# Performance work log

Measured on AMD Instinct MI355X. Metric: run time of the kernel, lower is better.

## Reference

```python
import jax, jax.numpy as jnp
import numpy as np

N = 50000; E = 800000
GNN_IN = 256; MLP_IN = 256; HID = 512; F_DIM = 128; H = 2; NCLS = 40
HC = H * F_DIM  # 256


def setup_inputs() -> dict:
    key = jax.random.key(0)
    ks = jax.random.split(key, 24)
    w = lambda k, shape: (jax.random.normal(k, shape, jnp.float32) * 0.05)
    inp = {
        'x_gsage': jax.random.normal(ks[0], (N, GNN_IN), jnp.float32),
        'edge_index': jax.random.randint(ks[1], (2, E), 0, N),
        'x_mlp': jax.random.normal(ks[2], (N, MLP_IN), jnp.float32),
        # TransformerConv params (query/key/value/skip linears)
        'Wq': w(ks[3], (HC, GNN_IN)), 'bq': jnp.zeros(HC, jnp.float32),
        'Wk': w(ks[4], (HC, GNN_IN)), 'bk': jnp.zeros(HC, jnp.float32),
        'Wv': w(ks[5], (HC, GNN_IN)), 'bv': jnp.zeros(HC, jnp.float32),
        'Wskip': w(ks[6], (HC, GNN_IN)), 'bskip': jnp.zeros(HC, jnp.float32),
        # MLP (num_layers=3): in->hid, hid->hid, hid->2*F_DIM; 2 batchnorms
        'W1': w(ks[7], (HID, MLP_IN)), 'b1': jnp.zeros(HID, jnp.float32),
        'g1': jnp.ones(HID, jnp.float32), 'be1': jnp.zeros(HID, jnp.float32),
        'W2': w(ks[8], (HID, HID)), 'b2': jnp.zeros(HID, jnp.float32),
        'g2': jnp.ones(HID, jnp.float32), 'be2': jnp.zeros(HID, jnp.float32),
        'W3': w(ks[9], (HC, HID)), 'b3': jnp.zeros(HC, jnp.float32),
        # fusion scalars
        'alpha': jnp.array([0.5], jnp.float32), 'beta': jnp.array([0.5], jnp.float32),
        # classifier head
        'Wc1': w(ks[10], (HID, HC)), 'bc1': jnp.zeros(HID, jnp.float32),
        'Wc2': w(ks[11], (NCLS, HID)), 'bc2': jnp.zeros(NCLS, jnp.float32),
    }
    return inp


def _lin(x, W, b):
    return x @ W.T + b


def _batchnorm(x, g, b, eps=1e-5):
    mu = jnp.mean(x, axis=0)
    var = jnp.var(x, axis=0)
    return (x - mu) * jax.lax.rsqrt(var + eps) * g + b


def _transformer_conv(x, edge_index, Wq, bq, Wk, bk, Wv, bv, Wskip, bskip):
    # PyG TransformerConv, heads=H, concat=True, root_weight=True (eval: no dropout)
    q = _lin(x, Wq, bq).reshape(N, H, F_DIM)
    k = _lin(x, Wk, bk).reshape(N, H, F_DIM)
    v = _lin(x, Wv, bv).reshape(N, H, F_DIM)
    src, dst = edge_index[0], edge_index[1]
    # per-edge, per-head attention logits  [E, H]
    logits = jnp.einsum('ehd,ehd->eh', q[dst], k[src]) / jnp.sqrt(jnp.float32(F_DIM))
    # segment softmax over incoming edges of each destination node
    amax = jax.ops.segment_max(logits, dst, num_segments=N)  # [N, H]
    amax = jnp.where(jnp.isfinite(amax), amax, 0.0)
    ex = jnp.exp(logits - amax[dst])                           # [E, H]
    denom = jax.ops.segment_sum(ex, dst, num_segments=N)      # [N, H]
    attn = ex / jnp.maximum(denom[dst], 1e-16)                 # [E, H]
    msg = v[src] * attn[:, :, None]                            # [E, H, C]
    out = jax.ops.segment_sum(msg, dst, num_segments=N)       # [N, H, C]
    out = out.reshape(N, HC) + _lin(x, Wskip, bskip)
    return out


def reference(x_gsage, edge_index, x_mlp, Wq, bq, Wk, bk, Wv, bv, Wskip, bskip,
              W1, b1, g1, be1, W2, b2, g2, be2, W3, b3, alpha, beta,
              Wc1, bc1, Wc2, bc2):
    h_g = _transformer_conv(x_gsage, edge_index, Wq, bq, Wk, bk, Wv, bv, Wskip, bskip)
    # MLP branch: (lin -> BN(batch stats) -> sigmoid) x2, then final lin; dropout off (eval)
    h = jax.nn.sigmoid(_batchnorm(_lin(x_mlp, W1, b1), g1, be1))
    h = jax.nn.sigmoid(_batchnorm(_lin(h, W2, b2), g2, be2))
    h_m = _lin(h, W3, b3)
    h_fused = alpha * h_g + beta * h_m
    out = _lin(jax.nn.relu(_lin(h_fused, Wc1, bc1)), Wc2, bc2)
    return out
```

## Files before the change

kernel.cpp:

```cpp
#include <hip/hip_runtime.h>
#include <hip/hip_bf16.h>
#include <cstdint>
#include <cstddef>

typedef __attribute__((ext_vector_type(8))) short short8;
typedef __attribute__((ext_vector_type(4))) float f32x4;

__device__ inline ushort f2bs(float f) {
    __hip_bfloat16 h = __float2bfloat16(f);
    return *(ushort*)&h;
}
__device__ inline float bu2f(ushort u) {
    return __uint_as_float(((unsigned)u) << 16);
}

template <int AB, int BM, int KT>
__global__ __launch_bounds__(256) void gemm_fullk(
    const void* __restrict__ Avoid, const short* __restrict__ Wb,
    const float* __restrict__ bias, ushort* __restrict__ C,
    int M, int NT, int act)
{
    __shared__ short As[BM][KT + 8];
    __shared__ short Bs[128][40];

    const int tid = threadIdx.x;
    const int lane = tid & 63;
    const int w = tid >> 6;
    const int wm = w >> 1, wn = w & 1;
    constexpr int MI = BM / 32;
    const int m0 = blockIdx.x * BM;
    const int lr = lane & 15;
    const int lk = (lane >> 4) * 8;
    const int Ntot = NT * 128;

    {
        constexpr int TPR = KT / 128;
        const int arow = tid / TPR;
        const int ac0 = (tid % TPR) * 128;
        const bool ok = (m0 + arow) < M;
        if (AB == 0) {
            const float* ap = (const float*)Avoid + (size_t)(m0 + arow) * KT + ac0;
#pragma unroll
            for (int j = 0; j < 16; ++j) {
                float4 x = ok ? *(const float4*)(ap + j * 8)
                              : make_float4(0.f, 0.f, 0.f, 0.f);
                float4 y = ok ? *(const float4*)(ap + j * 8 + 4)
                              : make_float4(0.f, 0.f, 0.f, 0.f);
                short8 v;
                v[0] = f2bs(x.x); v[1] = f2bs(x.y); v[2] = f2bs(x.z); v[3] = f2bs(x.w);
                v[4] = f2bs(y.x); v[5] = f2bs(y.y); v[6] = f2bs(y.z); v[7] = f2bs(y.w);
                *(short8*)&As[arow][ac0 + j * 8] = v;
            }
        } else {
            const short* ap = (const short*)Avoid + (size_t)(m0 + arow) * KT + ac0;
#pragma unroll
            for (int j = 0; j < 16; ++j) {
                short8 v = {};
                if (ok) v = *(const short8*)(ap + j * 8);
                *(short8*)&As[arow][ac0 + j * 8] = v;
            }
        }
    }

    const int trow = tid >> 1;
    const int tcg = (tid & 1) * 16;

    f32x4 acc[MI][4] = {};

    for (int t = 0; t < NT; ++t) {
        for (int k0 = 0; k0 < KT; k0 += 32) {
            const short* wp = Wb + (size_t)(t * 128 + trow) * KT + k0 + tcg;
            *(short8*)&Bs[trow][tcg] = *(const short8*)wp;
            *(short8*)&Bs[trow][tcg + 8] = *(const short8*)(wp + 8);
            __syncthreads();

            short8 afr[MI], bfr[4];
#pragma unroll
            for (int mi = 0; mi < MI; ++mi)
                afr[mi] = *(const short8*)&As[wm * (BM / 2) + mi * 16 + lr][k0 + lk];
#pragma unroll
            for (int nj = 0; nj < 4; ++nj)
                bfr[nj] = *(const short8*)&Bs[wn * 64 + nj * 16 + lr][lk];
#pragma unroll
            for (int mi = 0; mi < MI; ++mi)
#pragma unroll
                for (int nj = 0; nj < 4; ++nj)
                    acc[mi][nj] = __builtin_amdgcn_mfma_f32_16x16x32_bf16(
                        afr[mi], bfr[nj], acc[mi][nj], 0, 0, 0);
            __syncthreads();
        }
#pragma unroll
        for (int mi = 0; mi < MI; ++mi) {
#pragma unroll
            for (int nj = 0; nj < 4; ++nj) {
                int gn = t * 128 + wn * 64 + nj * 16 + lr;
                float b = bias[gn];
#pragma unroll
                for (int r = 0; r < 4; ++r) {
                    int gm = m0 + wm * (BM / 2) + mi * 16 + (lane >> 4) * 4 + r;
                    if (gm < M) {
                        float v = acc[mi][nj][r] + b;
                        if (act == 1) v = fmaxf(v, 0.f);
                        C[(size_t)gm * Ntot + gn] = f2bs(v);
                    }
                }
                acc[mi][nj] = (f32x4){0.f, 0.f, 0.f, 0.f};
            }
        }
    }
}

__global__ __launch_bounds__(256) void mfma_gemm_small(
    const short* __restrict__ A, const float* __restrict__ W,
    const float* __restrict__ bias, float* __restrict__ Cf,
    int M, int K, int Nout)
{
    __shared__ short As[128][40];
    __shared__ short Bs[128][40];
    const int tid = threadIdx.x;
    const int lane = tid & 63;
    const int w = tid >> 6;
    const int wm = w >> 1, wn = w & 1;
    const int m0 = blockIdx.y * 128, n0 = blockIdx.x * 128;
    const int trow = tid >> 1;
    const int tcg = (tid & 1) * 16;
    const int lr = lane & 15;
    const int lk = (lane >> 4) * 8;

    f32x4 acc[4][4] = {};

    for (int k0 = 0; k0 < K; k0 += 32) {
        {
            bool ok = (m0 + trow) < M;
            const short* ap = A + (size_t)(m0 + trow) * K + k0 + tcg;
            short8 s0 = {}, s1 = {};
            if (ok) { s0 = *(const short8*)(ap); s1 = *(const short8*)(ap + 8); }
            *(short8*)&As[trow][tcg] = s0;
            *(short8*)&As[trow][tcg + 8] = s1;
        }
        {
            short v[16];
            bool ok = (n0 + trow) < Nout;
            const float* wp = W + (size_t)(n0 + trow) * K + k0 + tcg;
#pragma unroll
            for (int q = 0; q < 4; ++q) {
                float4 t4 = ok ? *(const float4*)(wp + q * 4)
                               : make_float4(0.f, 0.f, 0.f, 0.f);
                v[q * 4 + 0] = f2bs(t4.x); v[q * 4 + 1] = f2bs(t4.y);
                v[q * 4 + 2] = f2bs(t4.z); v[q * 4 + 3] = f2bs(t4.w);
            }
            short8 w0, w1;
#pragma unroll
            for (int j = 0; j < 8; ++j) { w0[j] = v[j]; w1[j] = v[j + 8]; }
            *(short8*)&Bs[trow][tcg] = w0;
            *(short8*)&Bs[trow][tcg + 8] = w1;
        }
        __syncthreads();
        short8 afr[4], bfr[4];
#pragma unroll
        for (int mi = 0; mi < 4; ++mi)
            afr[mi] = *(const short8*)&As[wm * 64 + mi * 16 + lr][lk];
#pragma unroll
        for (int nj = 0; nj < 4; ++nj)
            bfr[nj] = *(const short8*)&Bs[wn * 64 + nj * 16 + lr][lk];
#pragma unroll
        for (int mi = 0; mi < 4; ++mi)
#pragma unroll
            for (int nj = 0; nj < 4; ++nj)
                acc[mi][nj] = __builtin_amdgcn_mfma_f32_16x16x32_bf16(
                    afr[mi], bfr[nj], acc[mi][nj], 0, 0, 0);
        __syncthreads();
    }
#pragma unroll
    for (int mi = 0; mi < 4; ++mi)
#pragma unroll
        for (int nj = 0; nj < 4; ++nj) {
            int gn = n0 + wn * 64 + nj * 16 + lr;
            if (gn >= Nout) continue;
            float b = bias[gn];
#pragma unroll
            for (int r = 0; r < 4; ++r) {
                int gm = m0 + wm * 64 + mi * 16 + (lane >> 4) * 4 + r;
                if (gm < M) Cf[(size_t)gm * Nout + gn] = acc[mi][nj][r] + b;
            }
        }
}

__global__ void zero_words(unsigned* __restrict__ p, size_t n)
{
    size_t i = (size_t)blockIdx.x * blockDim.x + threadIdx.x;
    size_t stride = (size_t)gridDim.x * blockDim.x;
    for (; i < n; i += stride) p[i] = 0u;
}

__global__ void cvt_f32_bf16(const float* __restrict__ s, ushort* __restrict__ d,
                             size_t n4)
{
    size_t i = (size_t)blockIdx.x * blockDim.x + threadIdx.x;
    size_t stride = (size_t)gridDim.x * blockDim.x;
    for (; i < n4; i += stride) {
        float4 v = ((const float4*)s)[i];
        ushort4 o;
        o.x = f2bs(v.x); o.y = f2bs(v.y); o.z = f2bs(v.z); o.w = f2bs(v.w);
        ((ushort4*)d)[i] = o;
    }
}

__global__ void copy_f32(const float* __restrict__ s, float* __restrict__ d, int n)
{
    int i = blockIdx.x * blockDim.x + threadIdx.x;
    if (i < n) d[i] = s[i];
}

__global__ __launch_bounds__(256) void bn_stats512_b(
    const ushort* __restrict__ X, float* __restrict__ sums,
    float* __restrict__ sumsq, int M)
{
    int t = threadIdx.x;
    float s0 = 0.f, q0 = 0.f, s1 = 0.f, q1 = 0.f;
    for (int r = blockIdx.x; r < M; r += gridDim.x) {
        ushort2 v = *(const ushort2*)(X + (size_t)r * 512 + 2 * t);
        float a = bu2f(v.x), b = bu2f(v.y);
        s0 += a; q0 += a * a;
        s1 += b; q1 += b * b;
    }
    atomicAdd(&sums[2 * t], s0);
    atomicAdd(&sumsq[2 * t], q0);
    atomicAdd(&sums[2 * t + 1], s1);
    atomicAdd(&sumsq[2 * t + 1], q1);
}

__global__ void bn_finalize(const float* __restrict__ sums,
                            const float* __restrict__ sumsq,
                            const float* __restrict__ g,
                            const float* __restrict__ be,
                            float* __restrict__ scale, float* __restrict__ shift,
                            int M, int C)
{
    int c = blockIdx.x * blockDim.x + threadIdx.x;
    if (c >= C) return;
    float mean = sums[c] / (float)M;
    float var = sumsq[c] / (float)M - mean * mean;
    float inv = rsqrtf(var + 1e-5f);
    float sc = g[c] * inv;
    scale[c] = sc;
    shift[c] = be[c] - mean * sc;
}

__global__ void bn_apply_sig4(ushort* __restrict__ X,
                              const float* __restrict__ scale,
                              const float* __restrict__ shift, size_t n4)
{
    size_t i = (size_t)blockIdx.x * blockDim.x + threadIdx.x;
    size_t stride = (size_t)gridDim.x * blockDim.x;
    for (; i < n4; i += stride) {
        ushort4 v = ((ushort4*)X)[i];
        int c0 = (int)((i * 4) & 511);
        float x0 = bu2f(v.x) * scale[c0] + shift[c0];
        float x1 = bu2f(v.y) * scale[c0 + 1] + shift[c0 + 1];
        float x2 = bu2f(v.z) * scale[c0 + 2] + shift[c0 + 2];
        float x3 = bu2f(v.w) * scale[c0 + 3] + shift[c0 + 3];
        v.x = f2bs(1.f / (1.f + __expf(-x0)));
        v.y = f2bs(1.f / (1.f + __expf(-x1)));
        v.z = f2bs(1.f / (1.f + __expf(-x2)));
        v.w = f2bs(1.f / (1.f + __expf(-x3)));
        ((ushort4*)X)[i] = v;
    }
}

__global__ void count_edges(const int* __restrict__ ei, int* __restrict__ counts, int E)
{
    int i = blockIdx.x * 256 + threadIdx.x;
    if (i < E) atomicAdd(&counts[ei[E + i]], 1);
}

__global__ __launch_bounds__(256) void scan_local(
    const int* __restrict__ cnt, int* __restrict__ excl,
    int* __restrict__ bsums, int n)
{
    __shared__ int s[256];
    int t = threadIdx.x;
    int i = blockIdx.x * 256 + t;
    int v = (i < n) ? cnt[i] : 0;
    s[t] = v;
    __syncthreads();
    for (int off = 1; off < 256; off <<= 1) {
        int u = (t >= off) ? s[t - off] : 0;
        __syncthreads();
        s[t] += u;
        __syncthreads();
    }
    if (i < n) excl[i] = s[t] - v;
    if (t == 255) bsums[blockIdx.x] = s[255];
}

__global__ __launch_bounds__(256) void scan_top(int* __restrict__ bsums, int nb)
{
    __shared__ int s[256];
    int t = threadIdx.x;
    int v = (t < nb) ? bsums[t] : 0;
    s[t] = v;
    __syncthreads();
    for (int off = 1; off < 256; off <<= 1) {
        int u = (t >= off) ? s[t - off] : 0;
        __syncthreads();
        s[t] += u;
        __syncthreads();
    }
    if (t < nb) bsums[t] = s[t] - v;
}

__global__ void scan_add(int* __restrict__ excl, const int* __restrict__ bsums,
                         int* __restrict__ cursor, int n)
{
    int i = blockIdx.x * 256 + threadIdx.x;
    if (i < n) {
        int v = excl[i] + bsums[blockIdx.x];
        excl[i] = v;
        cursor[i] = v;
    }
}

__global__ void fill_edges(const int* __restrict__ ei, int* __restrict__ cursor,
                           int* __restrict__ esrc, int E)
{
    int i = blockIdx.x * 256 + threadIdx.x;
    if (i < E) {
        int dst = ei[E + i];
        int pos = atomicAdd(&cursor[dst], 1);
        esrc[pos] = ei[i];
    }
}

__global__ __launch_bounds__(256) void edge_attn(
    const int* __restrict__ esrc, const int* __restrict__ offs,
    const int* __restrict__ cnts, const ushort* __restrict__ QKVS,
    const ushort* __restrict__ hmb, const float* __restrict__ alpha,
    const float* __restrict__ beta, ushort* __restrict__ hf, int N)
{
    int node = blockIdx.x * 4 + (threadIdx.x >> 6);
    int lane = threadIdx.x & 63;
    if (node >= N) return;
    int start = offs[node];
    int cnt = cnts[node];

    ushort4 qu = *(const ushort4*)(QKVS + (size_t)node * 1024 + lane * 4);
    float qx = bu2f(qu.x), qy = bu2f(qu.y), qz = bu2f(qu.z), qw = bu2f(qu.w);
    const float s = 0.088388347648318447f;

    float m = -INFINITY, d = 0.f;
    float a0 = 0.f, a1 = 0.f, a2 = 0.f, a3 = 0.f;

    ushort4 ku_n = {}, vu_n = {};
    if (cnt > 0) {
        int src0 = esrc[start];
        ku_n = *(const ushort4*)(QKVS + (size_t)src0 * 1024 + 256 + lane * 4);
        vu_n = *(const ushort4*)(QKVS + (size_t)src0 * 1024 + 512 + lane * 4);
    }
    for (int i = 0; i < cnt; ++i) {
        ushort4 ku = ku_n, vu = vu_n;
        if (i + 1 < cnt) {
            int srcn = esrc[start + i + 1];
            ku_n = *(const ushort4*)(QKVS + (size_t)srcn * 1024 + 256 + lane * 4);
            vu_n = *(const ushort4*)(QKVS + (size_t)srcn * 1024 + 512 + lane * 4);
        }
        float p = qx * bu2f(ku.x) + qy * bu2f(ku.y)
                + qz * bu2f(ku.z) + qw * bu2f(ku.w);
        p += __shfl_xor(p, 1);
        p += __shfl_xor(p, 2);
        p += __shfl_xor(p, 4);
        p += __shfl_xor(p, 8);
        p += __shfl_xor(p, 16);
        float l = p * s;
        float mn = fmaxf(m, l);
        float sc = __expf(m - mn);
        float pe = __expf(l - mn);
        d = d * sc + pe;
        a0 = a0 * sc + pe * bu2f(vu.x);
        a1 = a1 * sc + pe * bu2f(vu.y);
        a2 = a2 * sc + pe * bu2f(vu.z);
        a3 = a3 * sc + pe * bu2f(vu.w);
        m = mn;
    }
    float invd = (cnt > 0) ? 1.f / fmaxf(d, 1e-16f) : 0.f;
    float o0 = a0 * invd, o1 = a1 * invd, o2 = a2 * invd, o3 = a3 * invd;

    ushort4 su = *(const ushort4*)(QKVS + (size_t)node * 1024 + 768 + lane * 4);
    ushort4 hm = *(const ushort4*)(hmb + (size_t)node * 256 + lane * 4);
    float al = alpha[0], be = beta[0];
    ushort4 o;
    o.x = f2bs(al * (o0 + bu2f(su.x)) + be * bu2f(hm.x));
    o.y = f2bs(al * (o1 + bu2f(su.y)) + be * bu2f(hm.y));
    o.z = f2bs(al * (o2 + bu2f(su.z)) + be * bu2f(hm.z));
    o.w = f2bs(al * (o3 + bu2f(su.w)) + be * bu2f(hm.w));
    *(ushort4*)(hf + (size_t)node * 256 + lane * 4) = o;
}

extern "C" void kernel_launch(void* const* d_in, const int* in_sizes, int n_in,
                              void* d_out, int out_size, void* d_ws, size_t ws_size,
                              hipStream_t stream)
{
    const float* x_g   = (const float*)d_in[0];
    const int*   ei    = (const int*)d_in[1];
    const float* x_m   = (const float*)d_in[2];
    const float* Wq    = (const float*)d_in[3];
    const float* bq    = (const float*)d_in[4];
    const float* Wk    = (const float*)d_in[5];
    const float* bk    = (const float*)d_in[6];
    const float* Wv    = (const float*)d_in[7];
    const float* bv    = (const float*)d_in[8];
    const float* Wskip = (const float*)d_in[9];
    const float* bskip = (const float*)d_in[10];
    const float* W1    = (const float*)d_in[11];
    const float* b1    = (const float*)d_in[12];
    const float* g1    = (const float*)d_in[13];
    const float* be1   = (const float*)d_in[14];
    const float* W2    = (const float*)d_in[15];
    const float* b2    = (const float*)d_in[16];
    const float* g2    = (const float*)d_in[17];
    const float* be2   = (const float*)d_in[18];
    const float* W3    = (const float*)d_in[19];
    const float* b3    = (const float*)d_in[20];
    const float* alpha = (const float*)d_in[21];
    const float* beta  = (const float*)d_in[22];
    const float* Wc1   = (const float*)d_in[23];
    const float* bc1   = (const float*)d_in[24];
    const float* Wc2   = (const float*)d_in[25];
    const float* bc2   = (const float*)d_in[26];
    float* out = (float*)d_out;

    const int N = in_sizes[0] / 256;
    const int E = in_sizes[1] / 2;

    float* ws = (float*)d_ws;
    ushort* QKVS = (ushort*)ws;
    ushort* bufA = (ushort*)(ws + (size_t)N * 512);
    ushort* bufB = (ushort*)(ws + (size_t)N * 512 + (size_t)N * 256);
    ushort* hmb  = (ushort*)(ws + (size_t)N * 512 + 2 * (size_t)N * 256);
    float* wz = ws + (size_t)N * 512 + 2 * (size_t)N * 256 + (size_t)N * 128;

    float* sum1 = wz, *sq1 = wz + 512, *sum2 = wz + 1024, *sq2 = wz + 1536;
    int* counts = (int*)(wz + 2048);
    float* wz2 = wz + 2048 + N;
    float* scale1 = wz2, *shift1 = wz2 + 512;
    float* scale2 = wz2 + 1024, *shift2 = wz2 + 1536;
    int* bsums = (int*)(wz2 + 2048);
    int* offs = bsums + 256;
    int* cursor = offs + N;
    int* esrc = cursor + N;
    short* Wcat = (short*)(esrc + E);
    float* bcat = (float*)(Wcat + 1024 * 256);
    short* W1b  = (short*)(bcat + 1024);
    short* W2b  = W1b + 512 * 256;
    short* W3b  = W2b + 512 * 512;
    short* Wc1b = W3b + 256 * 512;

    dim3 blk(256);
    auto cvt = [&](const float* s, short* d, size_t n) {
        size_t n4 = n / 4;
        int g = (int)((n4 + 255) / 256);
        if (g > 512) g = 512;
        hipLaunchKernelGGL(cvt_f32_bf16, dim3(g), blk, 0, stream, s, (ushort*)d, n4);
    };

    hipLaunchKernelGGL(zero_words, dim3(128), blk, 0, stream,
                       (unsigned*)wz, (size_t)(2048 + N));

    cvt(Wq, Wcat, 256 * 256);
    cvt(Wk, Wcat + 256 * 256, 256 * 256);
    cvt(Wv, Wcat + 512 * 256, 256 * 256);
    cvt(Wskip, Wcat + 768 * 256, 256 * 256);
    cvt(W1, W1b, 512 * 256);
    cvt(W2, W2b, 512 * 512);
    cvt(W3, W3b, 256 * 512);
    cvt(Wc1, Wc1b, 512 * 256);
    hipLaunchKernelGGL(copy_f32, dim3(1), blk, 0, stream, bq, bcat, 256);
    hipLaunchKernelGGL(copy_f32, dim3(1), blk, 0, stream, bk, bcat + 256, 256);
    hipLaunchKernelGGL(copy_f32, dim3(1), blk, 0, stream, bv, bcat + 512, 256);
    hipLaunchKernelGGL(copy_f32, dim3(1), blk, 0, stream, bskip, bcat + 768, 256);

    const int nb = (N + 255) / 256;
    hipLaunchKernelGGL(count_edges, dim3((E + 255) / 256), blk, 0, stream, ei, counts, E);
    hipLaunchKernelGGL(scan_local, dim3(nb), blk, 0, stream, counts, offs, bsums, N);
    hipLaunchKernelGGL(scan_top, dim3(1), blk, 0, stream, bsums, nb);
    hipLaunchKernelGGL(scan_add, dim3(nb), blk, 0, stream, offs, bsums, cursor, N);
    hipLaunchKernelGGL(fill_edges, dim3((E + 255) / 256), blk, 0, stream, ei, cursor, esrc, E);

    const int g128 = (N + 127) / 128;
    const int g64 = (N + 63) / 64;

    hipLaunchKernelGGL((gemm_fullk<0, 128, 256>), dim3(g128), blk, 0, stream,
                       x_m, W1b, b1, bufA, N, 4, 0);
    hipLaunchKernelGGL(bn_stats512_b, dim3(512), blk, 0, stream, bufA, sum1, sq1, N);
    hipLaunchKernelGGL(bn_finalize, dim3(2), blk, 0, stream, sum1, sq1, g1, be1, scale1, shift1, N, 512);
    hipLaunchKernelGGL(bn_apply_sig4, dim3(2048), blk, 0, stream, bufA, scale1, shift1, (size_t)N * 128);
    hipLaunchKernelGGL((gemm_fullk<1, 64, 512>), dim3(g64), blk, 0, stream,
                       bufA, W2b, b2, bufB, N, 4, 0);
    hipLaunchKernelGGL(bn_stats512_b, dim3(512), blk, 0, stream, bufB, sum2, sq2, N);
    hipLaunchKernelGGL(bn_finalize, dim3(2), blk, 0, stream, sum2, sq2, g2, be2, scale2, shift2, N, 512);
    hipLaunchKernelGGL(bn_apply_sig4, dim3(2048), blk, 0, stream, bufB, scale2, shift2, (size_t)N * 128);
    hipLaunchKernelGGL((gemm_fullk<1, 64, 512>), dim3(g64), blk, 0, stream,
                       bufB, W3b, b3, hmb, N, 2, 0);

    hipLaunchKernelGGL((gemm_fullk<0, 128, 256>), dim3(g128), blk, 0, stream,
                       x_g, Wcat, bcat, QKVS, N, 8, 0);

    hipLaunchKernelGGL(edge_attn, dim3((N + 3) / 4), blk, 0, stream,
                       esrc, offs, counts, QKVS, hmb, alpha, beta, bufA, N);

    hipLaunchKernelGGL((gemm_fullk<1, 128, 256>), dim3(g128), blk, 0, stream,
                       bufA, Wc1b, bc1, bufB, N, 4, 1);
    hipLaunchKernelGGL(mfma_gemm_small, dim3(1, (N + 127) / 128), blk, 0, stream,
                       (const short*)bufB, Wc2, bc2, out, N, 512, 40);
}
```

Measured before the change: 940.9 us.

## Fuse BN+sigmoid into GEMM A-load, prefetch weights, pack param conversion

Removes the two standalone batchnorm-apply+sigmoid passes by applying scale/shift and sigmoid while staging A tiles into shared memory in the following GEMM. The GEMM loop is flattened over N-tiles and K-chunks, and the next weight chunk is prefetched into registers before the MFMA work so global loads overlap compute. The many small weight-convert and bias-copy launches are merged into one pack_params kernel. This saves two full read-write passes over 50000x512 bf16 buffers plus several launches, at the cost of extra per-element exp work inside the GEMM A-load.

New measurement: 962.6 us. 1.02x slower.

```diff
diff --git a/kernel.cpp b/kernel.cpp
--- a/kernel.cpp
+++ b/kernel.cpp
@@ -14,12 +14,14 @@
     return __uint_as_float(((unsigned)u) << 16);
 }
 
-template <int AB, int BM, int KT>
+template <int AB, int BM, int KT, int SIG>
 __global__ __launch_bounds__(256) void gemm_fullk(
     const void* __restrict__ Avoid, const short* __restrict__ Wb,
     const float* __restrict__ bias, ushort* __restrict__ C,
+    const float* __restrict__ scale, const float* __restrict__ shift,
     int M, int NT, int act)
 {
+    constexpr int KQ = KT / 32;
     __shared__ short As[BM][KT + 8];
     __shared__ short Bs[128][40];
 
@@ -57,6 +59,14 @@
             for (int j = 0; j < 16; ++j) {
                 short8 v = {};
                 if (ok) v = *(const short8*)(ap + j * 8);
+                if (SIG) {
+#pragma unroll
+                    for (int e = 0; e < 8; ++e) {
+                        int c = ac0 + j * 8 + e;
+                        float f = bu2f((ushort)v[e]) * scale[c] + shift[c];
+                        v[e] = (short)f2bs(1.f / (1.f + __expf(-f)));
+                    }
+                }
                 *(short8*)&As[arow][ac0 + j * 8] = v;
             }
         }
@@ -65,46 +75,64 @@
     const int trow = tid >> 1;
     const int tcg = (tid & 1) * 16;
 
+    short8 r0, r1;
+    {
+        const short* wp = Wb + (size_t)trow * KT + tcg;
+        r0 = *(const short8*)wp;
+        r1 = *(const short8*)(wp + 8);
+    }
+
     f32x4 acc[MI][4] = {};
-
-    for (int t = 0; t < NT; ++t) {
-        for (int k0 = 0; k0 < KT; k0 += 32) {
-            const short* wp = Wb + (size_t)(t * 128 + trow) * KT + k0 + tcg;
-            *(short8*)&Bs[trow][tcg] = *(const short8*)wp;
-            *(short8*)&Bs[trow][tcg + 8] = *(const short8*)(wp + 8);
-            __syncthreads();
-
-            short8 afr[MI], bfr[4];
-#pragma unroll
-            for (int mi = 0; mi < MI; ++mi)
-                afr[mi] = *(const short8*)&As[wm * (BM / 2) + mi * 16 + lr][k0 + lk];
+    const int total = NT * KQ;
+
+    for (int idx = 0; idx < total; ++idx) {
+        *(short8*)&Bs[trow][tcg] = r0;
+        *(short8*)&Bs[trow][tcg + 8] = r1;
+        __syncthreads();
+
+        const int nidx = idx + 1;
+        if (nidx < total) {
+            const int nt = nidx / KQ, nk = (nidx % KQ) * 32;
+            const short* wp = Wb + (size_t)(nt * 128 + trow) * KT + nk + tcg;
+            r0 = *(const short8*)wp;
+            r1 = *(const short8*)(wp + 8);
+        }
+
+        const int k0 = (idx % KQ) * 32;
+        short8 afr[MI], bfr[4];
+#pragma unroll
+        for (int mi = 0; mi < MI; ++mi)
+            afr[mi] = *(const short8*)&As[wm * (BM / 2) + mi * 16 + lr][k0 + lk];
+#pragma unroll
+        for (int nj = 0; nj < 4; ++nj)
+            bfr[nj] = *(const short8*)&Bs[wn * 64 + nj * 16 + lr][lk];
+#pragma unroll
+        for (int mi = 0; mi < MI; ++mi)
 #pragma unroll
             for (int nj = 0; nj < 4; ++nj)
-                bfr[nj] = *(const short8*)&Bs[wn * 64 + nj * 16 + lr][lk];
-#pragma unroll
-            for (int mi = 0; mi < MI; ++mi)
-#pragma unroll
-                for (int nj = 0; nj < 4; ++nj)
-                    acc[mi][nj] = __builtin_amdgcn_mfma_f32_16x16x32_bf16(
-                        afr[mi], bfr[nj], acc[mi][nj], 0, 0, 0);
-            __syncthreads();
-        }
-#pragma unroll
-        for (int mi = 0; mi < MI; ++mi) {
-#pragma unroll
-            for (int nj = 0; nj < 4; ++nj) {
-                int gn = t * 128 + wn * 64 + nj * 16 + lr;
-                float b = bias[gn];
-#pragma unroll
-                for (int r = 0; r < 4; ++r) {
-                    int gm = m0 + wm * (BM / 2) + mi * 16 + (lane >> 4) * 4 + r;
-                    if (gm < M) {
-                        float v = acc[mi][nj][r] + b;
-                        if (act == 1) v = fmaxf(v, 0.f);
-                        C[(size_t)gm * Ntot + gn] = f2bs(v);
+                acc[mi][nj] = __builtin_amdgcn_mfma_f32_16x16x32_bf16(
+                    afr[mi], bfr[nj], acc[mi][nj], 0, 0, 0);
+        __syncthreads();
+
+        if ((idx % KQ) == KQ - 1) {
+            const int t = idx / KQ;
+#pragma unroll
+            for (int mi = 0; mi < MI; ++mi) {
+#pragma unroll
+                for (int nj = 0; nj < 4; ++nj) {
+                    int gn = t * 128 + wn * 64 + nj * 16 + lr;
+                    float b = bias[gn];
+#pragma unroll
+                    for (int r = 0; r < 4; ++r) {
+                        int gm = m0 + wm * (BM / 2) + mi * 16 + (lane >> 4) * 4 + r;
+                        if (gm < M) {
+                            float v = acc[mi][nj][r] + b;
+                            if (act == 1) v = fmaxf(v, 0.f);
+                            C[(size_t)gm * Ntot + gn] = f2bs(v);
+                        }
                     }
+                    acc[mi][nj] = (f32x4){0.f, 0.f, 0.f, 0.f};
                 }
-                acc[mi][nj] = (f32x4){0.f, 0.f, 0.f, 0.f};
             }
         }
     }
@@ -193,23 +221,35 @@
     for (; i < n; i += stride) p[i] = 0u;
 }
 
-__global__ void cvt_f32_bf16(const float* __restrict__ s, ushort* __restrict__ d,
-                             size_t n4)
-{
-    size_t i = (size_t)blockIdx.x * blockDim.x + threadIdx.x;
-    size_t stride = (size_t)gridDim.x * blockDim.x;
-    for (; i < n4; i += stride) {
-        float4 v = ((const float4*)s)[i];
+__global__ void pack_params(
+    const float* __restrict__ Wq, const float* __restrict__ Wk,
+    const float* __restrict__ Wv, const float* __restrict__ Wskip,
+    const float* __restrict__ W1, const float* __restrict__ W2,
+    const float* __restrict__ W3, const float* __restrict__ Wc1,
+    const float* __restrict__ bq, const float* __restrict__ bk,
+    const float* __restrict__ bv, const float* __restrict__ bskip,
+    ushort* __restrict__ Wall, float* __restrict__ bcat)
+{
+    int q = blockIdx.x * 256 + threadIdx.x;
+    if (q < 229376) {
+        const float* s; int base4;
+        if      (q < 16384)  { s = Wq;    base4 = 0; }
+        else if (q < 32768)  { s = Wk;    base4 = 16384; }
+        else if (q < 49152)  { s = Wv;    base4 = 32768; }
+        else if (q < 65536)  { s = Wskip; base4 = 49152; }
+        else if (q < 98304)  { s = W1;    base4 = 65536; }
+        else if (q < 163840) { s = W2;    base4 = 98304; }
+        else if (q < 196608) { s = W3;    base4 = 163840; }
+        else                 { s = Wc1;   base4 = 196608; }
+        float4 v = ((const float4*)s)[q - base4];
         ushort4 o;
         o.x = f2bs(v.x); o.y = f2bs(v.y); o.z = f2bs(v.z); o.w = f2bs(v.w);
-        ((ushort4*)d)[i] = o;
-    }
-}
-
-__global__ void copy_f32(const float* __restrict__ s, float* __restrict__ d, int n)
-{
-    int i = blockIdx.x * blockDim.x + threadIdx.x;
-    if (i < n) d[i] = s[i];
+        ((ushort4*)Wall)[q] = o;
+    } else if (q < 229632) {
+        int j = q - 229376;
+        const float* s = (j < 64) ? bq : (j < 128) ? bk : (j < 192) ? bv : bskip;
+        ((float4*)bcat)[j] = ((const float4*)s)[j & 63];
+    }
 }
 
 __global__ __launch_bounds__(256) void bn_stats512_b(
@@ -245,27 +285,6 @@
     float sc = g[c] * inv;
     scale[c] = sc;
     shift[c] = be[c] - mean * sc;
-}
-
-__global__ void bn_apply_sig4(ushort* __restrict__ X,
-                              const float* __restrict__ scale,
-                              const float* __restrict__ shift, size_t n4)
-{
-    size_t i = (size_t)blockIdx.x * blockDim.x + threadIdx.x;
-    size_t stride = (size_t)gridDim.x * blockDim.x;
-    for (; i < n4; i += stride) {
-        ushort4 v = ((ushort4*)X)[i];
-        int c0 = (int)((i * 4) & 511);
-        float x0 = bu2f(v.x) * scale[c0] + shift[c0];
-        float x1 = bu2f(v.y) * scale[c0 + 1] + shift[c0 + 1];
-        float x2 = bu2f(v.z) * scale[c0 + 2] + shift[c0 + 2];
-        float x3 = bu2f(v.w) * scale[c0 + 3] + shift[c0 + 3];
-        v.x = f2bs(1.f / (1.f + __expf(-x0)));
-        v.y = f2bs(1.f / (1.f + __expf(-x1)));
-        v.z = f2bs(1.f / (1.f + __expf(-x2)));
-        v.w = f2bs(1.f / (1.f + __expf(-x3)));
-        ((ushort4*)X)[i] = v;
-    }
 }
 
 __global__ void count_edges(const int* __restrict__ ei, int* __restrict__ counts, int E)
@@ -435,9 +454,9 @@
     float* ws = (float*)d_ws;
     ushort* QKVS = (ushort*)ws;
     ushort* bufA = (ushort*)(ws + (size_t)N * 512);
-    ushort* bufB = (ushort*)(ws + (size_t)N * 512 + (size_t)N * 256);
-    ushort* hmb  = (ushort*)(ws + (size_t)N * 512 + 2 * (size_t)N * 256);
-    float* wz = ws + (size_t)N * 512 + 2 * (size_t)N * 256 + (size_t)N * 128;
+    ushort* bufB = (ushort*)(ws + (size_t)N * 768);
+    ushort* hmb  = (ushort*)(ws + (size_t)N * 1024);
+    float* wz = ws + (size_t)N * 1152;
 
     float* sum1 = wz, *sq1 = wz + 512, *sum2 = wz + 1024, *sq2 = wz + 1536;
     int* counts = (int*)(wz + 2048);
@@ -448,36 +467,22 @@
     int* offs = bsums + 256;
     int* cursor = offs + N;
     int* esrc = cursor + N;
-    short* Wcat = (short*)(esrc + E);
-    float* bcat = (float*)(Wcat + 1024 * 256);
-    short* W1b  = (short*)(bcat + 1024);
-    short* W2b  = W1b + 512 * 256;
-    short* W3b  = W2b + 512 * 512;
-    short* Wc1b = W3b + 256 * 512;
+    short* Wall = (short*)(esrc + E);
+    float* bcat = (float*)(Wall + 917504);
+    const short* Wcat = Wall;
+    const short* W1b  = Wall + 262144;
+    const short* W2b  = Wall + 393216;
+    const short* W3b  = Wall + 655360;
+    const short* Wc1b = Wall + 786432;
 
     dim3 blk(256);
-    auto cvt = [&](const float* s, short* d, size_t n) {
-        size_t n4 = n / 4;
-        int g = (int)((n4 + 255) / 256);
-        if (g > 512) g = 512;
-        hipLaunchKernelGGL(cvt_f32_bf16, dim3(g), blk, 0, stream, s, (ushort*)d, n4);
-    };
 
     hipLaunchKernelGGL(zero_words, dim3(128), blk, 0, stream,
                        (unsigned*)wz, (size_t)(2048 + N));
 
-    cvt(Wq, Wcat, 256 * 256);
-    cvt(Wk, Wcat + 256 * 256, 256 * 256);
-    cvt(Wv, Wcat + 512 * 256, 256 * 256);
-    cvt(Wskip, Wcat + 768 * 256, 256 * 256);
-    cvt(W1, W1b, 512 * 256);
-    cvt(W2, W2b, 512 * 512);
-    cvt(W3, W3b, 256 * 512);
-    cvt(Wc1, Wc1b, 512 * 256);
-    hipLaunchKernelGGL(copy_f32, dim3(1), blk, 0, stream, bq, bcat, 256);
-    hipLaunchKernelGGL(copy_f32, dim3(1), blk, 0, stream, bk, bcat + 256, 256);
-    hipLaunchKernelGGL(copy_f32, dim3(1), blk, 0, stream, bv, bcat + 512, 256);
-    hipLaunchKernelGGL(copy_f32, dim3(1), blk, 0, stream, bskip, bcat + 768, 256);
+    hipLaunchKernelGGL(pack_params, dim3(898), blk, 0, stream,
+                       Wq, Wk, Wv, Wskip, W1, W2, W3, Wc1,
+                       bq, bk, bv, bskip, (ushort*)Wall, bcat);
 
     const int nb = (N + 255) / 256;
     hipLaunchKernelGGL(count_edges, dim3((E + 255) / 256), blk, 0, stream, ei, counts, E);
@@ -489,27 +494,25 @@
     const int g128 = (N + 127) / 128;
     const int g64 = (N + 63) / 64;
 
-    hipLaunchKernelGGL((gemm_fullk<0, 128, 256>), dim3(g128), blk, 0, stream,
-                       x_m, W1b, b1, bufA, N, 4, 0);
+    hipLaunchKernelGGL((gemm_fullk<0, 128, 256, 0>), dim3(g128), blk, 0, stream,
+                       x_m, W1b, b1, bufA, nullptr, nullptr, N, 4, 0);
     hipLaunchKernelGGL(bn_stats512_b, dim3(512), blk, 0, stream, bufA, sum1, sq1, N);
     hipLaunchKernelGGL(bn_finalize, dim3(2), blk, 0, stream, sum1, sq1, g1, be1, scale1, shift1, N, 512);
-    hipLaunchKernelGGL(bn_apply_sig4, dim3(2048), blk, 0, stream, bufA, scale1, shift1, (size_t)N * 128);
-    hipLaunchKernelGGL((gemm_fullk<1, 64, 512>), dim3(g64), blk, 0, stream,
-                       bufA, W2b, b2, bufB, N, 4, 0);
+    hipLaunchKernelGGL((gemm_fullk<1, 64, 512, 1>), dim3(g64), blk, 0, stream,
+                       bufA, W2b, b2, bufB, scale1, shift1, N, 4, 0);
     hipLaunchKernelGGL(bn_stats512_b, dim3(512), blk, 0, stream, bufB, sum2, sq2, N);
     hipLaunchKernelGGL(bn_finalize, dim3(2), blk, 0, stream, sum2, sq2, g2, be2, scale2, shift2, N, 512);
-    hipLaunchKernelGGL(bn_apply_sig4, dim3(2048), blk, 0, stream, bufB, scale2, shift2, (size_t)N * 128);
-    hipLaunchKernelGGL((gemm_fullk<1, 64, 512>), dim3(g64), blk, 0, stream,
-                       bufB, W3b, b3, hmb, N, 2, 0);
-
-    hipLaunchKernelGGL((gemm_fullk<0, 128, 256>), dim3(g128), blk, 0, stream,
-                       x_g, Wcat, bcat, QKVS, N, 8, 0);
+    hipLaunchKernelGGL((gemm_fullk<1, 64, 512, 1>), dim3(g64), blk, 0, stream,
+                       bufB, W3b, b3, hmb, scale2, shift2, N, 2, 0);
+
+    hipLaunchKernelGGL((gemm_fullk<0, 128, 256, 0>), dim3(g128), blk, 0, stream,
+                       x_g, Wcat, bcat, QKVS, nullptr, nullptr, N, 8, 0);
 
     hipLaunchKernelGGL(edge_attn, dim3((N + 3) / 4), blk, 0, stream,
                        esrc, offs, counts, QKVS, hmb, alpha, beta, bufA, N);
 
-    hipLaunchKernelGGL((gemm_fullk<1, 128, 256>), dim3(g128), blk, 0, stream,
-                       bufA, Wc1b, bc1, bufB, N, 4, 1);
+    hipLaunchKernelGGL((gemm_fullk<1, 128, 256, 0>), dim3(g128), blk, 0, stream,
+                       bufA, Wc1b, bc1, bufB, nullptr, nullptr, N, 4, 1);
     hipLaunchKernelGGL(mfma_gemm_small, dim3(1, (N + 127) / 128), blk, 0, stream,
                        (const short*)bufB, Wc2, bc2, out, N, 512, 40);
 }
```
